# Kernel tuning notes

Measured on AMD Instinct MI355X. Metric: run time of the kernel, lower is better.

## Reference

```python
import jax, jax.numpy as jnp
import numpy as np

TEMPERATURE = 0.5
BATCH_SIZE = 4096
EPS = 1e-8  # torch.nn.CosineSimilarity default eps


def setup_inputs() -> dict:
    key = jax.random.key(0)
    k1, k2 = jax.random.split(key)
    z1 = jax.random.normal(k1, (BATCH_SIZE, 256), dtype=jnp.float32)
    z2 = jax.random.normal(k2, (BATCH_SIZE, 256), dtype=jnp.float32)
    return {"z1": z1, "z2": z2}


def reference(z1, z2):
    B = z1.shape[0]
    N = 2 * B
    reps = jnp.concatenate([z1, z2], axis=0)  # [N, D]
    # Cosine similarity (torch clamps each norm to eps before dividing)
    norms = jnp.maximum(jnp.linalg.norm(reps, axis=1, keepdims=True), EPS)
    z = reps / norms
    sim = z @ z.T  # [N, N] cosine similarity matrix

    # positives: diagonals at offsets +B and -B (they are identical by symmetry,
    # but keep the original concat order: [diag(+B), diag(-B)])
    l_pos = jnp.diagonal(sim, offset=B)
    r_pos = jnp.diagonal(sim, offset=-B)
    positives = jnp.concatenate([l_pos, r_pos])  # [N]

    inv_t = 1.0 / TEMPERATURE
    pos_logit = positives * inv_t  # logits[:, 0]

    # negatives are all off-diagonal entries of each row (the positive pair is
    # thus present twice in the logits, faithful to the original). CE with
    # label 0 => loss_i = logsumexp(logits_i) - logits_i[0].
    neg_logits = jnp.where(jnp.eye(N, dtype=bool), -jnp.inf, sim * inv_t)
    lse = jnp.logaddexp(pos_logit, jax.scipy.special.logsumexp(neg_logits, axis=1))
    loss = jnp.sum(lse - pos_logit) / N
    return loss
```

## Files before the change

### kernel.cpp

```cpp
#include <hip/hip_runtime.h>
#include <hip/hip_bf16.h>
#include <cstdint>
#include <cstddef>
#include <math.h>

#define BSZ   4096
#define NROW  8192
#define DIM   256
#define INV_T 2.0f
#define EPS_N 1e-8f

typedef __attribute__((ext_vector_type(8))) short bf16x8;
typedef __attribute__((ext_vector_type(4))) float f32x4;

__device__ __forceinline__ unsigned short f2bf(float x) {
    __hip_bfloat16 h = __float2bfloat16(x);
    return __builtin_bit_cast(unsigned short, h);
}

__device__ __forceinline__ void load_lds16(const void* g, void* l) {
    __builtin_amdgcn_global_load_lds(
        (const __attribute__((address_space(1))) void*)g,
        (__attribute__((address_space(3))) void*)l,
        16, 0, 0);
}

__global__ __launch_bounds__(256)
void nt_normalize(const float* __restrict__ z1,
                  const float* __restrict__ z2,
                  char* __restrict__ zn2,
                  float* __restrict__ rowsum) {
    const int wave = threadIdx.x >> 6;
    const int lane = threadIdx.x & 63;
    const int row  = blockIdx.x * 4 + wave;
    const float* src = (row < BSZ) ? (z1 + (size_t)row * DIM)
                                   : (z2 + (size_t)(row - BSZ) * DIM);
    const float4 v = ((const float4*)src)[lane];
    float ss = v.x * v.x + v.y * v.y + v.z * v.z + v.w * v.w;
    #pragma unroll
    for (int off = 32; off; off >>= 1) ss += __shfl_xor(ss, off);
    const float rinv = 1.0f / fmaxf(sqrtf(ss), EPS_N);
    ushort4 o;
    o.x = f2bf(v.x * rinv);
    o.y = f2bf(v.y * rinv);
    o.z = f2bf(v.z * rinv);
    o.w = f2bf(v.w * rinv);
    const int s    = row >> 7;
    const int lrow = row & 127;
    const int kc   = lane >> 4;
    const int unit = (lane >> 1) & 7;
    const int half = lane & 1;
    const int u    = unit ^ (lrow & 7);
    *(ushort4*)(zn2 + (size_t)s * 65536 + kc * 16384 + lrow * 128 + u * 16 + half * 8) = o;
    if (lane == 0) rowsum[row] = 0.0f;
}

__global__ __launch_bounds__(256)
void nt_gram(const char* __restrict__ zn2,
             float* __restrict__ rowsum,
             float* __restrict__ pos) {
    const int l = blockIdx.x;
    int bi = (int)((129.0 - sqrt(16641.0 - 8.0 * (double)l)) * 0.5);
    while (64 * (bi + 1) - (bi + 1) * bi / 2 <= l) ++bi;
    while (64 * bi - bi * (bi - 1) / 2 > l) --bi;
    const int bj = bi + (l - (64 * bi - bi * (bi - 1) / 2));

    __shared__ char As[16384];
    __shared__ char Bs[16384];

    const int t    = threadIdx.x;
    const int lane = t & 63;
    const int wave = t >> 6;
    const int wrow = (wave >> 1) * 64;
    const int wcol = (wave & 1) * 64;
    const int q    = lane >> 4;
    const int r16  = lane & 15;
    const int sw   = r16 & 7;

    const char* A2 = zn2 + (size_t)bi * 65536;
    const char* B2 = zn2 + (size_t)bj * 65536;

    f32x4 acc[4][4] = {};

    for (int kc = 0; kc < 4; ++kc) {
        #pragma unroll
        for (int p = 0; p < 4; ++p)
            load_lds16(A2 + kc * 16384 + p * 4096 + t * 16, As + p * 4096 + t * 16);
        #pragma unroll
        for (int p = 0; p < 4; ++p)
            load_lds16(B2 + kc * 16384 + p * 4096 + t * 16, Bs + p * 4096 + t * 16);
        __syncthreads();

        #pragma unroll
        for (int kk = 0; kk < 64; kk += 32) {
            const int cc   = (kk >> 3) + q;
            const int cpos = (cc ^ sw) << 4;
            bf16x8 af[4], bfr[4];
            #pragma unroll
            for (int mi = 0; mi < 4; ++mi)
                af[mi] = *(const bf16x8*)(As + (wrow + mi * 16 + r16) * 128 + cpos);
            #pragma unroll
            for (int ni = 0; ni < 4; ++ni)
                bfr[ni] = *(const bf16x8*)(Bs + (wcol + ni * 16 + r16) * 128 + cpos);
            #pragma unroll
            for (int mi = 0; mi < 4; ++mi)
                #pragma unroll
                for (int ni = 0; ni < 4; ++ni)
                    acc[mi][ni] = __builtin_amdgcn_mfma_f32_16x16x32_bf16(
                        af[mi], bfr[ni], acc[mi][ni], 0, 0, 0);
        }
        __syncthreads();
    }

    const int c = r16;
    const bool diag_block = (bi == bj);
    float colp[4] = {0.f, 0.f, 0.f, 0.f};

    #pragma unroll
    for (int mi = 0; mi < 4; ++mi) {
        #pragma unroll
        for (int r = 0; r < 4; ++r) {
            const int grow = bi * 128 + wrow + mi * 16 + q * 4 + r;
            float s = 0.f;
            #pragma unroll
            for (int ni = 0; ni < 4; ++ni) {
                const int gcol = bj * 128 + wcol + ni * 16 + c;
                const float val = acc[mi][ni][r];
                float e = __expf(val * INV_T);
                e = (grow == gcol) ? 0.f : e;
                s += e;
                colp[ni] += e;
                if (gcol == grow + BSZ) {
                    pos[grow] = val;
                    pos[gcol] = val;
                }
            }
            s += __shfl_xor(s, 1);
            s += __shfl_xor(s, 2);
            s += __shfl_xor(s, 4);
            s += __shfl_xor(s, 8);
            if (c == 0) atomicAdd(&rowsum[grow], s);
        }
    }
    if (!diag_block) {
        #pragma unroll
        for (int ni = 0; ni < 4; ++ni) {
            float cs = colp[ni];
            cs += __shfl_xor(cs, 16);
            cs += __shfl_xor(cs, 32);
            if (q == 0) atomicAdd(&rowsum[bj * 128 + wcol + ni * 16 + c], cs);
        }
    }
}

__global__ __launch_bounds__(1024)
void nt_finalize(const float* __restrict__ rowsum,
                 const float* __restrict__ pos,
                 float* __restrict__ out) {
    float v = 0.f;
    for (int i = threadIdx.x; i < NROW; i += 1024) {
        const float pl = pos[i] * INV_T;
        v += logf(__expf(pl) + rowsum[i]) - pl;
    }
    #pragma unroll
    for (int off = 32; off; off >>= 1) v += __shfl_xor(v, off);
    __shared__ float red[16];
    if ((threadIdx.x & 63) == 0) red[threadIdx.x >> 6] = v;
    __syncthreads();
    if (threadIdx.x == 0) {
        float s = 0.f;
        #pragma unroll
        for (int w = 0; w < 16; ++w) s += red[w];
        out[0] = s * (1.0f / NROW);
    }
}

extern "C" void kernel_launch(void* const* d_in, const int* in_sizes, int n_in,
                              void* d_out, int out_size, void* d_ws, size_t ws_size,
                              hipStream_t stream) {
    const float* z1 = (const float*)d_in[0];
    const float* z2 = (const float*)d_in[1];
    float* out = (float*)d_out;

    char*  zn2    = (char*)d_ws;
    float* rowsum = (float*)((char*)d_ws + (size_t)NROW * DIM * 2);
    float* pos    = rowsum + NROW;

    nt_normalize<<<NROW / 4, 256, 0, stream>>>(z1, z2, zn2, rowsum);
    nt_gram<<<2080, 256, 0, stream>>>(zn2, rowsum, pos);
    nt_finalize<<<1, 1024, 0, stream>>>(rowsum, pos, out);
}
```

Measured before the change: 107.2 us.

## Load A fragments directly from global into registers, skip A LDS staging

```diff
diff --git a/kernel.cpp b/kernel.cpp
--- a/kernel.cpp
+++ b/kernel.cpp
@@ -65,7 +65,6 @@
     while (64 * bi - bi * (bi - 1) / 2 > l) --bi;
     const int bj = bi + (l - (64 * bi - bi * (bi - 1) / 2));
 
-    __shared__ char As[16384];
     __shared__ char Bs[16384];
 
     const int t    = threadIdx.x;
@@ -76,6 +75,7 @@
     const int q    = lane >> 4;
     const int r16  = lane & 15;
     const int sw   = r16 & 7;
+    const int t16  = t * 16;
 
     const char* A2 = zn2 + (size_t)bi * 65536;
     const char* B2 = zn2 + (size_t)bj * 65536;
@@ -85,29 +85,32 @@
     for (int kc = 0; kc < 4; ++kc) {
         #pragma unroll
         for (int p = 0; p < 4; ++p)
-            load_lds16(A2 + kc * 16384 + p * 4096 + t * 16, As + p * 4096 + t * 16);
-        #pragma unroll
-        for (int p = 0; p < 4; ++p)
-            load_lds16(B2 + kc * 16384 + p * 4096 + t * 16, Bs + p * 4096 + t * 16);
+            load_lds16(B2 + kc * 16384 + p * 4096 + t16, Bs + p * 4096 + t16);
+
+        bf16x8 af[2][4];
+        #pragma unroll
+        for (int kh = 0; kh < 2; ++kh) {
+            const int cpos = (((kh << 2) + q) ^ sw) << 4;
+            #pragma unroll
+            for (int mi = 0; mi < 4; ++mi)
+                af[kh][mi] = *(const bf16x8*)(
+                    A2 + kc * 16384 + (wrow + mi * 16 + r16) * 128 + cpos);
+        }
         __syncthreads();
 
         #pragma unroll
-        for (int kk = 0; kk < 64; kk += 32) {
-            const int cc   = (kk >> 3) + q;
-            const int cpos = (cc ^ sw) << 4;
-            bf16x8 af[4], bfr[4];
-            #pragma unroll
-            for (int mi = 0; mi < 4; ++mi)
-                af[mi] = *(const bf16x8*)(As + (wrow + mi * 16 + r16) * 128 + cpos);
+        for (int kh = 0; kh < 2; ++kh) {
+            const int cpos = (((kh << 2) + q) ^ sw) << 4;
+            bf16x8 bfv[4];
             #pragma unroll
             for (int ni = 0; ni < 4; ++ni)
-                bfr[ni] = *(const bf16x8*)(Bs + (wcol + ni * 16 + r16) * 128 + cpos);
+                bfv[ni] = *(const bf16x8*)(Bs + (wcol + ni * 16 + r16) * 128 + cpos);
             #pragma unroll
             for (int mi = 0; mi < 4; ++mi)
                 #pragma unroll
                 for (int ni = 0; ni < 4; ++ni)
                     acc[mi][ni] = __builtin_amdgcn_mfma_f32_16x16x32_bf16(
-                        af[mi], bfr[ni], acc[mi][ni], 0, 0, 0);
+                        af[kh][mi], bfv[ni], acc[mi][ni], 0, 0, 0);
         }
         __syncthreads();
     }
@@ -157,20 +160,28 @@
 void nt_finalize(const float* __restrict__ rowsum,
                  const float* __restrict__ pos,
                  float* __restrict__ out) {
+    const float4* rs4 = (const float4*)rowsum;
+    const float4* ps4 = (const float4*)pos;
     float v = 0.f;
-    for (int i = threadIdx.x; i < NROW; i += 1024) {
-        const float pl = pos[i] * INV_T;
-        v += logf(__expf(pl) + rowsum[i]) - pl;
+    #pragma unroll
+    for (int it = 0; it < 2; ++it) {
+        const int i = it * 1024 + threadIdx.x;
+        const float4 r = rs4[i];
+        const float4 p = ps4[i];
+        v += logf(__expf(p.x * INV_T) + r.x) - p.x * INV_T;
+        v += logf(__expf(p.y * INV_T) + r.y) - p.y * INV_T;
+        v += logf(__expf(p.z * INV_T) + r.z) - p.z * INV_T;
+        v += logf(__expf(p.w * INV_T) + r.w) - p.w * INV_T;
     }
     #pragma unroll
     for (int off = 32; off; off >>= 1) v += __shfl_xor(v, off);
-    __shared__ float red[16];
-    if ((threadIdx.x & 63) == 0) red[threadIdx.x >> 6] = v;
+    __shared__ float redf[16];
+    if ((threadIdx.x & 63) == 0) redf[threadIdx.x >> 6] = v;
     __syncthreads();
     if (threadIdx.x == 0) {
         float s = 0.f;
         #pragma unroll
-        for (int w = 0; w < 16; ++w) s += red[w];
+        for (int w = 0; w < 16; ++w) s += redf[w];
         out[0] = s * (1.0f / NROW);
     }
 }
```

Measured after the change: 109.5 us. 1.02x slower.
